# Optimization experiments

Measured on AMD Instinct MI355X. Metric: run time of the kernel, lower is better.

## Reference

```python
import jax, jax.numpy as jnp
import numpy as np
from jax import lax

T_LEN, BATCH, IN_DIM, HID = 1024, 64, 256, 256


def setup_inputs() -> dict:
    key = jax.random.key(0)
    k1, k2, k3, k4 = jax.random.split(key, 4)
    x = jax.random.normal(k1, (T_LEN, BATCH, IN_DIM), dtype=jnp.float32)
    m = jax.random.normal(k2, (T_LEN, BATCH, HID), dtype=jnp.float32)
    h0 = jnp.zeros((BATCH, HID), dtype=jnp.float32)
    c0 = jnp.zeros((BATCH, HID), dtype=jnp.float32)
    # 5 gates: input, forget, cell, output, reinstatement
    scale = 1.0 / np.sqrt(HID)
    W_ih = jax.random.normal(k3, (5 * HID, IN_DIM), dtype=jnp.float32) * scale
    W_hh = jax.random.normal(k4, (5 * HID, HID), dtype=jnp.float32) * scale
    b = jnp.zeros((5 * HID,), dtype=jnp.float32)
    return {"x": x, "m": m, "h0": h0, "c0": c0, "W_ih": W_ih, "W_hh": W_hh, "b": b}


def reference(x, m, h0, c0, W_ih, W_hh, b):
    """Episodic LSTM: sequential scan over time (batch_first=False, forward direction).

    x: [T, B, I], m: [T, B, H] (retrieved episodic cell states per step).
    Returns (sequence [T, B, H], h_T [B, H], c_T [B, H]).
    """
    # Precompute input projections for all timesteps in one GEMM: [T, B, 5H]
    x_proj = jnp.einsum("tbi,gi->tbg", x, W_ih) + b

    def step(carry, inp):
        h, c = carry
        xp_t, m_t = inp
        gates = xp_t + h @ W_hh.T  # [B, 5H]
        i, f, g, o, r = jnp.split(gates, 5, axis=-1)
        c = (jax.nn.sigmoid(f) * c
             + jax.nn.sigmoid(i) * jnp.tanh(g)
             + jax.nn.sigmoid(r) * m_t)
        h = jax.nn.sigmoid(o) * jnp.tanh(c)
        return (h, c), h

    (hT, cT), seq = lax.scan(step, (h0, c0), (x_proj, m))
    return seq, hT, cT
```

## Files before the change

### kernel.cpp

```cpp
#include <hip/hip_runtime.h>
#include <stdint.h>
#include <stddef.h>

#define T_LEN 1024
#define BATCH 64
#define KDIM  256
#define HID   256
#define NGATE 5
#define GROWS (NGATE * HID)
#define NGT   (GROWS / 16)
#define NSWG  4

typedef __attribute__((ext_vector_type(8))) short s16x8;
typedef __attribute__((ext_vector_type(4))) float f32x4;
typedef __attribute__((ext_vector_type(4))) int   i32x4;
typedef __attribute__((ext_vector_type(2))) unsigned int u32x2;

static __device__ __forceinline__ uint16_t f2bf(float f) {
  uint32_t u = __float_as_uint(f);
  return (uint16_t)((u + 0x7fffu + ((u >> 16) & 1u)) >> 16);
}
static __device__ __forceinline__ float bf2f(uint16_t b) {
  return __uint_as_float(((uint32_t)b) << 16);
}
static __device__ __forceinline__ s16x8 cvt8(const float* __restrict__ p) {
  float4 a = *reinterpret_cast<const float4*>(p);
  float4 b = *reinterpret_cast<const float4*>(p + 4);
  union { s16x8 v; uint16_t u[8]; } r;
  r.u[0] = f2bf(a.x); r.u[1] = f2bf(a.y); r.u[2] = f2bf(a.z); r.u[3] = f2bf(a.w);
  r.u[4] = f2bf(b.x); r.u[5] = f2bf(b.y); r.u[6] = f2bf(b.z); r.u[7] = f2bf(b.w);
  return r.v;
}
static __device__ __forceinline__ float sigm(float x)   { return 1.f / (1.f + __expf(-x)); }
static __device__ __forceinline__ float tanh_f(float x) { return 1.f - 2.f / (__expf(2.f * x) + 1.f); }
static __device__ __forceinline__ int swz(int row, int col) {
  return ((((col >> 4) ^ (row & 15)) << 4) | (col & 15));
}

__global__ void setup_kernel(const float* __restrict__ Wih, const float* __restrict__ c0,
                             uint16_t* __restrict__ wihb, float* __restrict__ cbuf) {
  int i = blockIdx.x * 256 + threadIdx.x;
  if (i < GROWS * KDIM) wihb[i] = f2bf(Wih[i]);
  if (i < BATCH * HID) cbuf[i] = c0[i];
}

__global__ void wquant_kernel(const float* __restrict__ Whh,
                              int8_t* __restrict__ wq, float* __restrict__ wsc) {
  int row = blockIdx.x * 256 + threadIdx.x;
  if (row >= GROWS) return;
  const float* wr = Whh + (size_t)row * KDIM;
  float mx = 1e-30f;
  for (int k = 0; k < KDIM; ++k) mx = fmaxf(mx, fabsf(wr[k]));
  wsc[row] = mx / 127.f;
  const float inv = 127.f / mx;
  int8_t* q = wq + (size_t)row * KDIM;
  for (int k = 0; k < KDIM; ++k) q[k] = (int8_t)__float2int_rn(wr[k] * inv);
}

__global__ __launch_bounds__(256, 2)
void xproj_kernel(const float* __restrict__ x, const uint16_t* __restrict__ wihb,
                  const float* __restrict__ bias, uint16_t* __restrict__ xp, int t0) {
  const int w = threadIdx.x >> 6, lane = threadIdx.x & 63;
  const int r16 = lane & 15, ke = (lane >> 4) * 8;
  const int tA = t0 + (int)blockIdx.x * 2;

  s16x8 A[2][8];
#pragma unroll
  for (int tt = 0; tt < 2; ++tt) {
    const float* ap = x + ((size_t)(tA + tt) * BATCH + w * 16 + r16) * KDIM + ke;
#pragma unroll
    for (int ks = 0; ks < 8; ++ks) A[tt][ks] = cvt8(ap + ks * 32);
  }
  for (int gt = 0; gt < NGT; ++gt) {
    const uint16_t* bp = wihb + (size_t)(gt * 16 + r16) * KDIM + ke;
    s16x8 B[8];
#pragma unroll
    for (int ks = 0; ks < 8; ++ks) B[ks] = *reinterpret_cast<const s16x8*>(bp + ks * 32);
    const float bv = bias[gt * 16 + r16];
#pragma unroll
    for (int tt = 0; tt < 2; ++tt) {
      f32x4 acc = {};
#pragma unroll
      for (int ks = 0; ks < 8; ++ks)
        acc = __builtin_amdgcn_mfma_f32_16x16x32_bf16(A[tt][ks], B[ks], acc, 0, 0, 0);
      const int lt = (int)blockIdx.x * 2 + tt;
      uint32_t w0 = (uint32_t)f2bf(acc[0] + bv) | ((uint32_t)f2bf(acc[1] + bv) << 16);
      uint32_t w1 = (uint32_t)f2bf(acc[2] + bv) | ((uint32_t)f2bf(acc[3] + bv) << 16);
      u32x2 pk = {w0, w1};
      u32x2* dst = (u32x2*)((uint32_t*)(xp + ((size_t)(lt * 4 + w) * NGT + gt) * 256) + lane * 2);
      __builtin_nontemporal_store(pk, dst);
    }
  }
}

__global__ __launch_bounds__(1024, 4)
void scan_kernel(const float* __restrict__ mIn, const int8_t* __restrict__ wq,
                 const float* __restrict__ wsc, const uint16_t* __restrict__ xp,
                 const float* __restrict__ h_src, float* __restrict__ cbuf,
                 float* __restrict__ seq, float* __restrict__ hT, float* __restrict__ cT,
                 int s0, int s1) {
  struct SW {
    int8_t w[16][2][4][1024];
    int8_t hq[2][16][256];
  };
  __shared__ SW sl;
  const int wg = blockIdx.x;
  const int v = threadIdx.x >> 6;
  const int lane = threadIdx.x & 63;
  const int r16 = lane & 15, g4 = lane >> 4;
  const int bj0 = g4 * 4;
  const int brow = wg * 16;
  const int col = v * 16 + r16;

  i32x4 Wf[3][4];
  float sc[NGATE];
#pragma unroll
  for (int g = 0; g < NGATE; ++g) {
    const int grow = g * 256 + col;
    if (g < 3) {
      const int8_t* wp = wq + (size_t)grow * KDIM + g4 * 16;
#pragma unroll
      for (int ks = 0; ks < 4; ++ks)
        Wf[g][ks] = *reinterpret_cast<const i32x4*>(wp + ks * 64);
    }
    sc[g] = wsc[grow] * (1.f / 127.f);
  }
#pragma unroll
  for (int gl = 0; gl < 2; ++gl) {
    const int grow = (3 + gl) * 256 + col;
    const int8_t* wp = wq + (size_t)grow * KDIM + g4 * 16;
#pragma unroll
    for (int ks = 0; ks < 4; ++ks)
      *reinterpret_cast<i32x4*>(&sl.w[v][gl][ks][lane * 16]) =
          *reinterpret_cast<const i32x4*>(wp + ks * 64);
  }

  float c[4];
#pragma unroll
  for (int j = 0; j < 4; ++j)
    c[j] = cbuf[(size_t)(brow + bj0 + j) * HID + col];

  {
    const int p0 = s0 & 1;
#pragma unroll
    for (int e = 0; e < 4; ++e) {
      int t = (int)threadIdx.x * 4 + e;
      int row = t >> 8, cc = t & 255;
      float hv = h_src[(size_t)(brow + row) * HID + cc];
      int q = __float2int_rn(fminf(fmaxf(hv * 127.f, -127.f), 127.f));
      sl.hq[p0][row][swz(row, cc)] = (int8_t)q;
    }
  }
  __syncthreads();

  const uint16_t* xpb = xp + ((size_t)wg * NGT + v) * 256 + lane * 4;
  const float*    mb  = mIn + ((size_t)s0 * BATCH + brow + bj0) * HID + col;
  float*          sqb = seq + ((size_t)s0 * BATCH + brow + bj0) * HID + col;

  u32x2 xpf[NGATE];
  float mv[4];
#pragma unroll
  for (int g = 0; g < NGATE; ++g)
    xpf[g] = *reinterpret_cast<const u32x2*>(xpb + g * 16 * 256);
#pragma unroll
  for (int j = 0; j < 4; ++j) mv[j] = mb[j * HID];

  for (int s = s0; s < s1; ++s) {
    const int p = s & 1;

    i32x4 acc[NGATE] = {};
    __builtin_amdgcn_s_setprio(1);
#pragma unroll
    for (int ks = 0; ks < 4; ++ks) {
      i32x4 A = *reinterpret_cast<const i32x4*>(&sl.hq[p][r16][swz(r16, (g4 + 4 * ks) * 16)]);
      acc[0] = __builtin_amdgcn_mfma_i32_16x16x64_i8(A, Wf[0][ks], acc[0], 0, 0, 0);
      acc[1] = __builtin_amdgcn_mfma_i32_16x16x64_i8(A, Wf[1][ks], acc[1], 0, 0, 0);
      acc[2] = __builtin_amdgcn_mfma_i32_16x16x64_i8(A, Wf[2][ks], acc[2], 0, 0, 0);
      i32x4 b0 = *reinterpret_cast<const i32x4*>(&sl.w[v][0][ks][lane * 16]);
      acc[3] = __builtin_amdgcn_mfma_i32_16x16x64_i8(A, b0, acc[3], 0, 0, 0);
      i32x4 b1 = *reinterpret_cast<const i32x4*>(&sl.w[v][1][ks][lane * 16]);
      acc[4] = __builtin_amdgcn_mfma_i32_16x16x64_i8(A, b1, acc[4], 0, 0, 0);
    }
    __builtin_amdgcn_s_setprio(0);

    float hnew[4];
#pragma unroll
    for (int j = 0; j < 4; ++j) {
#define XPV(g) bf2f((uint16_t)((j & 1) ? (xpf[g][j >> 1] >> 16) : (xpf[g][j >> 1] & 0xffff)))
      const float gi = (float)acc[0][j] * sc[0] + XPV(0);
      const float gf = (float)acc[1][j] * sc[1] + XPV(1);
      const float gg = (float)acc[2][j] * sc[2] + XPV(2);
      const float go = (float)acc[3][j] * sc[3] + XPV(3);
      const float gr = (float)acc[4][j] * sc[4] + XPV(4);
#undef XPV
      const float cn = sigm(gf) * c[j] + sigm(gi) * tanh_f(gg) + sigm(gr) * mv[j];
      c[j] = cn;
      hnew[j] = sigm(go) * tanh_f(cn);
    }

    const uint16_t* xpb_n = xpb + 4 * NGT * 256;
    const float*    mb_n  = (s + 1 < s1) ? mb + BATCH * HID : mb;
#pragma unroll
    for (int g = 0; g < NGATE; ++g)
      xpf[g] = *reinterpret_cast<const u32x2*>(xpb_n + g * 16 * 256);
#pragma unroll
    for (int j = 0; j < 4; ++j) mv[j] = mb_n[j * HID];
    xpb = xpb_n; mb = mb_n;

#pragma unroll
    for (int j = 0; j < 4; ++j) {
      __builtin_nontemporal_store(hnew[j], sqb + j * HID);
      int q = __float2int_rn(hnew[j] * 127.f);
      sl.hq[p ^ 1][bj0 + j][swz(bj0 + j, col)] = (int8_t)q;
    }
    if (s == T_LEN - 1) {
#pragma unroll
      for (int j = 0; j < 4; ++j) {
        hT[(size_t)(brow + bj0 + j) * HID + col] = hnew[j];
        cT[(size_t)(brow + bj0 + j) * HID + col] = c[j];
      }
    }
    sqb += BATCH * HID;

    __builtin_amdgcn_sched_barrier(0);
    asm volatile("s_waitcnt lgkmcnt(0)" ::: "memory");
    __builtin_amdgcn_s_barrier();
    __builtin_amdgcn_sched_barrier(0);
  }

#pragma unroll
  for (int j = 0; j < 4; ++j)
    cbuf[(size_t)(brow + bj0 + j) * HID + col] = c[j];
}

extern "C" void kernel_launch(void* const* d_in, const int* in_sizes, int n_in,
                              void* d_out, int out_size, void* d_ws, size_t ws_size,
                              hipStream_t stream) {
  (void)in_sizes; (void)n_in; (void)out_size;
  const float* x    = (const float*)d_in[0];
  const float* mIn  = (const float*)d_in[1];
  const float* h0   = (const float*)d_in[2];
  const float* c0   = (const float*)d_in[3];
  const float* Wih  = (const float*)d_in[4];
  const float* Whh  = (const float*)d_in[5];
  const float* bias = (const float*)d_in[6];
  float* out = (float*)d_out;
  float* seq = out;
  float* hT  = out + (size_t)T_LEN * BATCH * HID;
  float* cT  = hT + (size_t)BATCH * HID;

  const size_t fixed = (size_t)GROWS * KDIM * 2 + (size_t)GROWS * KDIM
                     + (size_t)GROWS * 4 + (size_t)BATCH * HID * 4 + 4096;
  int tchunk = T_LEN;
  while (tchunk > 2 && (size_t)tchunk * BATCH * GROWS * 2 + fixed > ws_size) tchunk >>= 1;

  char* p = (char*)d_ws;
  uint16_t* xp   = (uint16_t*)p;  p += (size_t)tchunk * BATCH * GROWS * 2;
  uint16_t* wihb = (uint16_t*)p;  p += (size_t)GROWS * KDIM * 2;
  int8_t*   wq   = (int8_t*)p;    p += (size_t)GROWS * KDIM;
  float*    wsc  = (float*)p;     p += (size_t)GROWS * 4;
  float*    cbuf = (float*)p;

  setup_kernel<<<dim3((GROWS * KDIM + 255) / 256), dim3(256), 0, stream>>>(
      Wih, c0, wihb, cbuf);
  wquant_kernel<<<dim3((GROWS + 255) / 256), dim3(256), 0, stream>>>(Whh, wq, wsc);
  for (int s0 = 0; s0 < T_LEN; s0 += tchunk) {
    xproj_kernel<<<dim3(tchunk / 2), dim3(256), 0, stream>>>(x, wihb, bias, xp, s0);
    const float* h_src = (s0 == 0) ? h0 : (seq + (size_t)(s0 - 1) * BATCH * HID);
    scan_kernel<<<dim3(NSWG), dim3(1024), 0, stream>>>(
        mIn, wq, wsc, xp, h_src, cbuf, seq, hT, cT, s0, s0 + tchunk);
  }
}
```

Measured before the change: 4.004 ms.

## Use hardware rcp, inline-asm MFMA with AGPR weights, hoisted LDS offsets

Replaces the IEEE division in sigmoid/tanh with the hardware v_rcp_f32 approximation and makes the gate pre-activations explicit FMAs. The int8 MFMAs become inline asm so the register-resident weights and accumulators live in AGPRs, which frees VGPRs. Swizzled LDS read and write offsets are precomputed once outside the time loop instead of being recomputed every step. The intent is to shorten the serial per-step critical path of the recurrence, with slightly lower accuracy from the approximate reciprocal and the risk that AGPR/VGPR moves around the asm constraints add copies.

```diff
diff --git a/kernel.cpp b/kernel.cpp
--- a/kernel.cpp
+++ b/kernel.cpp
@@ -31,11 +31,23 @@
   r.u[4] = f2bf(b.x); r.u[5] = f2bf(b.y); r.u[6] = f2bf(b.z); r.u[7] = f2bf(b.w);
   return r.v;
 }
-static __device__ __forceinline__ float sigm(float x)   { return 1.f / (1.f + __expf(-x)); }
-static __device__ __forceinline__ float tanh_f(float x) { return 1.f - 2.f / (__expf(2.f * x) + 1.f); }
+static __device__ __forceinline__ float rcp_hw(float x) {
+  float r; asm("v_rcp_f32 %0, %1" : "=v"(r) : "v"(x)); return r;
+}
+static __device__ __forceinline__ float sigm(float x) {
+  return rcp_hw(1.f + __expf(-x));
+}
+static __device__ __forceinline__ float tanh_f(float x) {
+  return __builtin_fmaf(-2.f, rcp_hw(1.f + __expf(2.f * x)), 1.f);
+}
 static __device__ __forceinline__ int swz(int row, int col) {
   return ((((col >> 4) ^ (row & 15)) << 4) | (col & 15));
 }
+
+#define MFMA_AW(acc, A, W) \
+  asm("v_mfma_i32_16x16x64_i8 %0, %1, %2, %0" : "+a"(acc) : "v"(A), "a"(W))
+#define MFMA_AV(acc, A, B) \
+  asm("v_mfma_i32_16x16x64_i8 %0, %1, %2, %0" : "+a"(acc) : "v"(A), "v"(B))
 
 __global__ void setup_kernel(const float* __restrict__ Wih, const float* __restrict__ c0,
                              uint16_t* __restrict__ wihb, float* __restrict__ cbuf) {
@@ -112,18 +124,20 @@
   const int brow = wg * 16;
   const int col = v * 16 + r16;
 
-  i32x4 Wf[3][4];
+  i32x4 Wf0[4], Wf1[4], Wf2[4];
   float sc[NGATE];
 #pragma unroll
-  for (int g = 0; g < NGATE; ++g) {
-    const int grow = g * 256 + col;
-    if (g < 3) {
-      const int8_t* wp = wq + (size_t)grow * KDIM + g4 * 16;
-#pragma unroll
-      for (int ks = 0; ks < 4; ++ks)
-        Wf[g][ks] = *reinterpret_cast<const i32x4*>(wp + ks * 64);
-    }
-    sc[g] = wsc[grow] * (1.f / 127.f);
+  for (int g = 0; g < NGATE; ++g) sc[g] = wsc[g * 256 + col] * (1.f / 127.f);
+  {
+    const int8_t* wp0 = wq + (size_t)(0 * 256 + col) * KDIM + g4 * 16;
+    const int8_t* wp1 = wq + (size_t)(1 * 256 + col) * KDIM + g4 * 16;
+    const int8_t* wp2 = wq + (size_t)(2 * 256 + col) * KDIM + g4 * 16;
+#pragma unroll
+    for (int ks = 0; ks < 4; ++ks) {
+      Wf0[ks] = *reinterpret_cast<const i32x4*>(wp0 + ks * 64);
+      Wf1[ks] = *reinterpret_cast<const i32x4*>(wp1 + ks * 64);
+      Wf2[ks] = *reinterpret_cast<const i32x4*>(wp2 + ks * 64);
+    }
   }
 #pragma unroll
   for (int gl = 0; gl < 2; ++gl) {
@@ -153,6 +167,12 @@
   }
   __syncthreads();
 
+  int aoff[4], woff[4];
+#pragma unroll
+  for (int ks = 0; ks < 4; ++ks) aoff[ks] = r16 * 256 + swz(r16, (g4 + 4 * ks) * 16);
+#pragma unroll
+  for (int j = 0; j < 4; ++j) woff[j] = (bj0 + j) * 256 + swz(bj0 + j, col);
+
   const uint16_t* xpb = xp + ((size_t)wg * NGT + v) * 256 + lane * 4;
   const float*    mb  = mIn + ((size_t)s0 * BATCH + brow + bj0) * HID + col;
   float*          sqb = seq + ((size_t)s0 * BATCH + brow + bj0) * HID + col;
@@ -165,21 +185,27 @@
 #pragma unroll
   for (int j = 0; j < 4; ++j) mv[j] = mb[j * HID];
 
+  int8_t* const hq0 = &sl.hq[0][0][0];
+
   for (int s = s0; s < s1; ++s) {
     const int p = s & 1;
-
-    i32x4 acc[NGATE] = {};
+    const int8_t* hr = hq0 + p * 4096;
+    int8_t*       hw = hq0 + (p ^ 1) * 4096;
+
+    i32x4 acc[NGATE];
+#pragma unroll
+    for (int g = 0; g < NGATE; ++g) acc[g] = i32x4{0, 0, 0, 0};
     __builtin_amdgcn_s_setprio(1);
 #pragma unroll
     for (int ks = 0; ks < 4; ++ks) {
-      i32x4 A = *reinterpret_cast<const i32x4*>(&sl.hq[p][r16][swz(r16, (g4 + 4 * ks) * 16)]);
-      acc[0] = __builtin_amdgcn_mfma_i32_16x16x64_i8(A, Wf[0][ks], acc[0], 0, 0, 0);
-      acc[1] = __builtin_amdgcn_mfma_i32_16x16x64_i8(A, Wf[1][ks], acc[1], 0, 0, 0);
-      acc[2] = __builtin_amdgcn_mfma_i32_16x16x64_i8(A, Wf[2][ks], acc[2], 0, 0, 0);
+      i32x4 A = *reinterpret_cast<const i32x4*>(hr + aoff[ks]);
+      MFMA_AW(acc[0], A, Wf0[ks]);
+      MFMA_AW(acc[1], A, Wf1[ks]);
+      MFMA_AW(acc[2], A, Wf2[ks]);
       i32x4 b0 = *reinterpret_cast<const i32x4*>(&sl.w[v][0][ks][lane * 16]);
-      acc[3] = __builtin_amdgcn_mfma_i32_16x16x64_i8(A, b0, acc[3], 0, 0, 0);
+      MFMA_AV(acc[3], A, b0);
       i32x4 b1 = *reinterpret_cast<const i32x4*>(&sl.w[v][1][ks][lane * 16]);
-      acc[4] = __builtin_amdgcn_mfma_i32_16x16x64_i8(A, b1, acc[4], 0, 0, 0);
+      MFMA_AV(acc[4], A, b1);
     }
     __builtin_amdgcn_s_setprio(0);
 
@@ -187,11 +213,11 @@
 #pragma unroll
     for (int j = 0; j < 4; ++j) {
 #define XPV(g) bf2f((uint16_t)((j & 1) ? (xpf[g][j >> 1] >> 16) : (xpf[g][j >> 1] & 0xffff)))
-      const float gi = (float)acc[0][j] * sc[0] + XPV(0);
-      const float gf = (float)acc[1][j] * sc[1] + XPV(1);
-      const float gg = (float)acc[2][j] * sc[2] + XPV(2);
-      const float go = (float)acc[3][j] * sc[3] + XPV(3);
-      const float gr = (float)acc[4][j] * sc[4] + XPV(4);
+      const float gi = __builtin_fmaf((float)acc[0][j], sc[0], XPV(0));
+      const float gf = __builtin_fmaf((float)acc[1][j], sc[1], XPV(1));
+      const float gg = __builtin_fmaf((float)acc[2][j], sc[2], XPV(2));
+      const float go = __builtin_fmaf((float)acc[3][j], sc[3], XPV(3));
+      const float gr = __builtin_fmaf((float)acc[4][j], sc[4], XPV(4));
 #undef XPV
       const float cn = sigm(gf) * c[j] + sigm(gi) * tanh_f(gg) + sigm(gr) * mv[j];
       c[j] = cn;
@@ -211,7 +237,7 @@
     for (int j = 0; j < 4; ++j) {
       __builtin_nontemporal_store(hnew[j], sqb + j * HID);
       int q = __float2int_rn(hnew[j] * 127.f);
-      sl.hq[p ^ 1][bj0 + j][swz(bj0 + j, col)] = (int8_t)q;
+      hw[woff[j]] = (int8_t)q;
     }
     if (s == T_LEN - 1) {
 #pragma unroll
```

After: 3.643 ms. 9.0% less time.
